# Performance work log

Hardware: AMD Instinct MI355X
Metric: run time of the kernel (lower is better)

## Reference

```python
import jax, jax.numpy as jnp
import numpy as np

H = 1024
B, S = 4, 2048
SCALE = 1.0 / np.sqrt(H)  # single-head: head_dim == hidden_dim


def setup_inputs() -> dict:
    key = jax.random.key(0)
    k1, k2, k3, k4 = jax.random.split(key, 4)
    inp = jax.random.normal(k1, (B, S, H), dtype=jnp.float32)
    # nn.Linear(h, h, bias=False) weights, stored [out, in]
    wq = jax.random.normal(k2, (H, H), dtype=jnp.float32) / np.sqrt(H)
    wk = jax.random.normal(k3, (H, H), dtype=jnp.float32) / np.sqrt(H)
    wv = jax.random.normal(k4, (H, H), dtype=jnp.float32) / np.sqrt(H)
    # causal mask, broadcast over batch: 1 = attend, 0 = masked
    attention_mask = jnp.broadcast_to(
        jnp.tril(jnp.ones((S, S), dtype=jnp.int32)), (B, S, S))
    return {"input": inp, "attention_mask": attention_mask,
            "wq": wq, "wk": wk, "wv": wv}


def reference(input, attention_mask, wq, wk, wv):
    # Linear: x @ W^T
    Q = jnp.einsum('bsh,oh->bso', input, wq)
    K = jnp.einsum('bsh,oh->bso', input, wk)
    V = jnp.einsum('bsh,oh->bso', input, wv)
    scores = jnp.einsum('bqh,bkh->bqk', Q, K) * SCALE  # [B,S,S]
    neg_inf = jnp.asarray(-jnp.inf, dtype=scores.dtype)
    scores = jnp.where(attention_mask == 0, neg_inf, scores)
    attn = jax.nn.softmax(scores, axis=-1)
    # dropout prob = 0.0 (eval): identity
    return jnp.einsum('bqk,bkh->bqh', attn, V)
```

## Files before the change

### kernel.cpp

```cpp
#include <hip/hip_runtime.h>
#include <hip/hip_bf16.h>
#include <stdint.h>

typedef __attribute__((ext_vector_type(8))) short short8;
typedef __attribute__((ext_vector_type(4))) float f32x4;
typedef __attribute__((ext_vector_type(4))) float fvec4;
typedef __attribute__((ext_vector_type(4))) unsigned short us4;

#define DEV static __device__ __forceinline__

constexpr int Hn = 1024;
constexpr int Bn = 4;
constexpr int Sn = 2048;
constexpr float SCALE_F = 0.03125f;
constexpr float LOG2E_F = 1.4426950408889634f;
constexpr float CEXP = SCALE_F * LOG2E_F;
constexpr int PTILES = 136;

DEV unsigned short f2bf(float f) {
  union { float f; unsigned u; } c; c.f = f;
  unsigned r = c.u + 0x7fffu + ((c.u >> 16) & 1u);
  return (unsigned short)(r >> 16);
}

DEV void gload16(const void* g, void* l) {
  __builtin_amdgcn_global_load_lds(
      (const __attribute__((address_space(1))) void*)g,
      (__attribute__((address_space(3))) void*)l, 16, 0, 0);
}

#define VMCNT(n) asm volatile("s_waitcnt vmcnt(" #n ")" ::: "memory")
#define LGKM0()  asm volatile("s_waitcnt lgkmcnt(0)" ::: "memory")
#define BAR()    asm volatile("s_barrier" ::: "memory")

DEV int swz_wg(int bid, int n) {
  const int q = n >> 3, r = n & 7, x = bid & 7, o = bid >> 3;
  return (x < r ? x * (q + 1) : r * (q + 1) + (x - r) * q) + o;
}

__global__ __launch_bounds__(256) void cvt_kernel(
    const float* __restrict__ x, const float* __restrict__ wq,
    const float* __restrict__ wk, const float* __restrict__ wv,
    unsigned short* __restrict__ xb, unsigned short* __restrict__ wb,
    float* __restrict__ lz) {
  if (blockIdx.x == 0) {
    f32x4 z = {0.f, 0.f, 0.f, 0.f};
    for (int i = threadIdx.x; i < Bn * Sn / 4; i += 256) ((f32x4*)lz)[i] = z;
  }
  const int NX4 = Bn * Sn * Hn / 4;
  const int NW4 = Hn * Hn / 4;
  const int total = NX4 + 3 * NW4;
  for (int i = blockIdx.x * 256 + threadIdx.x; i < total; i += gridDim.x * 256) {
    const fvec4* s; us4* d; int j;
    if (i < NX4)                { s = (const fvec4*)x;  d = (us4*)xb;             j = i; }
    else if (i < NX4 + NW4)     { s = (const fvec4*)wq; d = (us4*)wb;             j = i - NX4; }
    else if (i < NX4 + 2 * NW4) { s = (const fvec4*)wk; d = (us4*)(wb + Hn * Hn); j = i - NX4 - NW4; }
    else                        { s = (const fvec4*)wv; d = (us4*)(wb + 2 * Hn * Hn); j = i - NX4 - 2 * NW4; }
    fvec4 v = s[j];
    us4 o;
    o[0] = f2bf(v[0]); o[1] = f2bf(v[1]); o[2] = f2bf(v[2]); o[3] = f2bf(v[3]);
    d[j] = o;
  }
}

#define MFMA16(H, V, B) do {                                                     \
  __builtin_amdgcn_s_setprio(1);                                                 \
  _Pragma("unroll") for (int m_ = 0; m_ < 4; m_++)                               \
  _Pragma("unroll") for (int n_ = 0; n_ < 2; n_++)                               \
  _Pragma("unroll") for (int ks_ = 0; ks_ < 2; ks_++)                            \
    acc[H][V][m_][n_] = __builtin_amdgcn_mfma_f32_16x16x32_bf16(                 \
        afr[m_][ks_], (B)[n_][ks_], acc[H][V][m_][n_], 0, 0, 0);                 \
  __builtin_amdgcn_s_setprio(0);                                                 \
  __builtin_amdgcn_sched_barrier(0);                                             \
} while (0)

template <int MODE>
__global__ __launch_bounds__(512, 2) void gemm256_kernel(
    const unsigned short* __restrict__ A, int lda, int64_t a_bstride,
    const unsigned short* __restrict__ Bm, int ldb, int64_t b_bstride,
    unsigned short* __restrict__ C0, unsigned short* __restrict__ C1,
    float* __restrict__ lsum, int n_split, int ldc, int bm_mod, int K) {
  __shared__ __attribute__((aligned(16))) unsigned short LDSm[8][8192];
  char* lds = (char*)LDSm;
  const int tid = threadIdx.x, lane = tid & 63, wave = tid >> 6;
  const int wr = wave >> 2, wc = wave & 3;
  const int ln15 = lane & 15, hi = lane >> 4;

  int bm, bn, zl = 0;
  const int wg = swz_wg(blockIdx.x, gridDim.x);
  if (MODE == 0) { bm = wg % bm_mod; bn = wg / bm_mod; }
  else {
    zl = wg / 36;
    const int t = wg - zl * 36;
    bm = (int)((sqrtf(8.f * t + 1.f) - 1.f) * 0.5f);
    if (bm * (bm + 1) / 2 > t) bm--;
    if ((bm + 1) * (bm + 2) / 2 <= t) bm++;
    bn = t - bm * (bm + 1) / 2;
  }
  const unsigned short* Ab = A + (int64_t)zl * a_bstride;
  const unsigned short* Bb = Bm + (int64_t)zl * b_bstride;

  const int srow = tid >> 3;
  const int kch = ((tid & 7) ^ (srow & 7)) << 3;
  const unsigned short* Ag = Ab + (int64_t)(bm * 256 + srow) * lda + kch;
  const unsigned short* Bg = Bb + (int64_t)(bn * 256 + srow) * ldb + kch;
  const int dst_off = tid * 16;

  auto stageA = [&](int half, int t, int buf) {
    const unsigned short* s = Ag + (int64_t)(half * 128) * lda + (t << 6);
    char* d = lds + ((buf * 4 + half) << 14) + dst_off;
    gload16(s, d);
    gload16(s + (int64_t)64 * lda, d + 8192);
  };
  auto stageB = [&](int half, int t, int buf) {
    const unsigned short* s = Bg + (int64_t)(half * 128) * ldb + (t << 6);
    char* d = lds + ((buf * 4 + 2 + half) << 14) + dst_off;
    gload16(s, d);
    gload16(s + (int64_t)64 * ldb, d + 8192);
  };
  auto rdA = [&](int buf, int half, int rr, int ks) -> short8 {
    return *(const short8*)(lds + ((buf * 4 + half) << 14) + rr * 128 +
                            (((ks << 6) + (hi << 4)) ^ ((rr & 7) << 4)));
  };
  auto rdB = [&](int buf, int half, int rr, int ks) -> short8 {
    return *(const short8*)(lds + ((buf * 4 + 2 + half) << 14) + rr * 128 +
                            (((ks << 6) + (hi << 4)) ^ ((rr & 7) << 4)));
  };

  f32x4 acc[2][2][4][2];
#pragma unroll
  for (int h = 0; h < 2; h++)
#pragma unroll
    for (int v = 0; v < 2; v++)
#pragma unroll
      for (int m = 0; m < 4; m++)
#pragma unroll
        for (int n = 0; n < 2; n++) acc[h][v][m][n] = (f32x4){0.f, 0.f, 0.f, 0.f};

  short8 afr[4][2], b0r[2][2], b1r[2][2];

  stageA(0, 0, 0); stageB(0, 0, 0); stageB(1, 0, 0); stageA(1, 0, 0);
  VMCNT(4);
  BAR();

  const int nkt = K >> 6;
  for (int t = 0; t < nkt; ++t) {
    const int buf = t & 1, nb2 = buf ^ 1;
    const bool st = (t + 1 < nkt);
#pragma unroll
    for (int m = 0; m < 4; m++) {
      afr[m][0] = rdA(buf, 0, wr * 64 + m * 16 + ln15, 0);
      afr[m][1] = rdA(buf, 0, wr * 64 + m * 16 + ln15, 1);
    }
#pragma unroll
    for (int n = 0; n < 2; n++) {
      b0r[n][0] = rdB(buf, 0, wc * 32 + n * 16 + ln15, 0);
      b0r[n][1] = rdB(buf, 0, wc * 32 + n * 16 + ln15, 1);
    }
    if (st) { stageA(0, t + 1, nb2); VMCNT(4); } else { VMCNT(2); }
    BAR(); LGKM0(); __builtin_amdgcn_sched_barrier(0);
    MFMA16(0, 0, b0r);
    BAR();
#pragma unroll
    for (int n = 0; n < 2; n++) {
      b1r[n][0] = rdB(buf, 1, wc * 32 + n * 16 + ln15, 0);
      b1r[n][1] = rdB(buf, 1, wc * 32 + n * 16 + ln15, 1);
    }
    if (st) { stageB(0, t + 1, nb2); VMCNT(4); } else { VMCNT(0); }
    BAR(); LGKM0(); __builtin_amdgcn_sched_barrier(0);
    MFMA16(0, 1, b1r);
    BAR();
#pragma unroll
    for (int m = 0; m < 4; m++) {
      afr[m][0] = rdA(buf, 1, wr * 64 + m * 16 + ln15, 0);
      afr[m][1] = rdA(buf, 1, wr * 64 + m * 16 + ln15, 1);
    }
    if (st) { stageB(1, t + 1, nb2); VMCNT(6); } else { VMCNT(0); }
    BAR(); LGKM0(); __builtin_amdgcn_sched_barrier(0);
    MFMA16(1, 0, b0r);
    BAR();
    if (st) { stageA(1, t + 1, nb2); VMCNT(4); } else { VMCNT(0); }
    BAR();
    MFMA16(1, 1, b1r);
    BAR();
  }

  if (MODE == 0) {
#pragma unroll
    for (int h = 0; h < 2; h++)
#pragma unroll
      for (int v = 0; v < 2; v++)
#pragma unroll
        for (int n = 0; n < 2; n++) {
          int cc = bn * 256 + v * 128 + wc * 32 + n * 16;
          unsigned short* cb = C0;
          if (cc >= n_split) { cb = C1; cc -= n_split; }
          cc += ln15;
#pragma unroll
          for (int m = 0; m < 4; m++) {
            const int r0 = bm * 256 + h * 128 + wr * 64 + m * 16 + hi * 4;
#pragma unroll
            for (int j = 0; j < 4; j++)
              cb[(int64_t)(r0 + j) * ldc + cc] = f2bf(acc[h][v][m][n][j]);
          }
        }
  } else {
    unsigned short* Pb = C0 + (int64_t)zl * (PTILES * 16384);
    float* lb = lsum + zl * Sn;
#pragma unroll
    for (int h = 0; h < 2; h++)
#pragma unroll
      for (int m = 0; m < 4; m++)
#pragma unroll
        for (int j = 0; j < 4; j++) {
          const int row = bm * 256 + h * 128 + wr * 64 + m * 16 + hi * 4 + j;
          const int tq = row >> 7;
          float s = 0.f;
#pragma unroll
          for (int v = 0; v < 2; v++)
#pragma unroll
            for (int n = 0; n < 2; n++) {
              const int col = bn * 256 + v * 128 + wc * 32 + n * 16 + ln15;
              const float p =
                  (col <= row) ? __builtin_amdgcn_exp2f(acc[h][v][m][n][j] * CEXP) : 0.f;
              s += p;
              const int tk = col >> 7;
              if (tk <= tq)
                Pb[((int64_t)(tq * (tq + 1) / 2 + tk) << 14) + ((row & 127) << 7) +
                   (col & 127)] = f2bf(p);
            }
          s += __shfl_xor(s, 1); s += __shfl_xor(s, 2);
          s += __shfl_xor(s, 4); s += __shfl_xor(s, 8);
          if (ln15 == 0) atomicAdd(&lb[row], s);
        }
  }
}

__global__ __launch_bounds__(256) void pv_gemm_kernel(
    const unsigned short* __restrict__ Pp,
    const unsigned short* __restrict__ VTb,
    const float* __restrict__ l,
    float* __restrict__ Out) {
  const int w = blockIdx.x;
  const int bm = 15 - (w >> 5);
  const int inner = w & 31;
  const int bn = inner & 7;
  const int b = inner >> 3;

  __shared__ __attribute__((aligned(16))) unsigned short As[2][128 * 32];
  __shared__ __attribute__((aligned(16))) unsigned short Bs[2][128 * 32];
  const int tid = threadIdx.x, lane = tid & 63, wave = tid >> 6;
  const int wr = wave >> 1, wc = wave & 1;
  const int ln15 = lane & 15, hi = lane >> 4;

  const int arow = wave * 32 + (lane >> 2);
  const int aswz = (((lane & 3) ^ ((lane >> 2) & 3)) << 3);
  const unsigned short* Abase = Pp + (int64_t)b * (PTILES * 16384) +
      ((int64_t)(bm * (bm + 1) / 2) << 14) + (arow << 7) + aswz;
  const unsigned short* Bg = VTb + (int64_t)(bn * 128 + arow) * (Bn * Sn) +
      (int64_t)b * Sn + aswz;

  f32x4 acc[4][4];
#pragma unroll
  for (int m = 0; m < 4; m++)
#pragma unroll
    for (int n = 0; n < 4; n++) acc[m][n] = (f32x4){0.f, 0.f, 0.f, 0.f};

  auto stage = [&](int kt, int buf) {
    const unsigned short* a_src = Abase + ((int64_t)(kt >> 2) << 14) + (kt & 3) * 32;
    const unsigned short* b_src = Bg + kt * 32;
    char* a = (char*)As[buf] + wave * 2048;
    char* bl = (char*)Bs[buf] + wave * 2048;
    gload16(a_src, a);
    gload16(a_src + 2048, a + 1024);
    gload16(b_src, bl);
    gload16(b_src + (int64_t)16 * (Bn * Sn), bl + 1024);
  };

  const int nkt = (bm + 1) * 4;
  stage(0, 0);
  __syncthreads();
  for (int kt = 0; kt < nkt; ++kt) {
    const int buf = kt & 1;
    if (kt + 1 < nkt) stage(kt + 1, buf ^ 1);
    const char* Ap = (const char*)As[buf];
    const char* Bp = (const char*)Bs[buf];
    short8 af[4], bfv[4];
#pragma unroll
    for (int m = 0; m < 4; m++) {
      const int rr = wr * 64 + m * 16 + ln15;
      af[m] = *(const short8*)(Ap + rr * 64 + ((hi ^ (rr & 3)) << 4));
    }
#pragma unroll
    for (int n = 0; n < 4; n++) {
      const int rr = wc * 64 + n * 16 + ln15;
      bfv[n] = *(const short8*)(Bp + rr * 64 + ((hi ^ (rr & 3)) << 4));
    }
#pragma unroll
    for (int m = 0; m < 4; m++)
#pragma unroll
      for (int n = 0; n < 4; n++)
        acc[m][n] = __builtin_amdgcn_mfma_f32_16x16x32_bf16(af[m], bfv[n], acc[m][n], 0, 0, 0);
    __syncthreads();
  }

#pragma unroll
  for (int m = 0; m < 4; m++) {
    const int r0 = bm * 128 + wr * 64 + m * 16 + hi * 4;
#pragma unroll
    for (int j = 0; j < 4; j++) {
      const int q = r0 + j;
      const float linv = 1.0f / l[(int64_t)b * Sn + q];
#pragma unroll
      for (int n = 0; n < 4; n++) {
        const int d = bn * 128 + wc * 64 + n * 16 + ln15;
        Out[(int64_t)b * Sn * Hn + (int64_t)q * Hn + d] = acc[m][n][j] * linv;
      }
    }
  }
}

extern "C" void kernel_launch(void* const* d_in, const int* in_sizes, int n_in,
                              void* d_out, int out_size, void* d_ws, size_t ws_size,
                              hipStream_t stream) {
  const float* x  = (const float*)d_in[0];
  const float* wq = (const float*)d_in[2];
  const float* wk = (const float*)d_in[3];
  const float* wv = (const float*)d_in[4];
  float* out = (float*)d_out;
  char* ws = (char*)d_ws;

  const int64_t MiB = 1ll << 20;
  unsigned short* xb = (unsigned short*)(ws);
  unsigned short* wb = (unsigned short*)(ws + 16 * MiB);
  unsigned short* Pp = (unsigned short*)(ws);
  float* l           = (float*)(ws + 22 * MiB);
  unsigned short* Qb = (unsigned short*)(ws + 23 * MiB);
  unsigned short* Kb = (unsigned short*)(ws + 39 * MiB);
  unsigned short* VT = (unsigned short*)(ws + 55 * MiB);

  cvt_kernel<<<2048, 256, 0, stream>>>(x, wq, wk, wv, xb, wb, l);
  gemm256_kernel<0><<<256, 512, 0, stream>>>(
      xb, 1024, 0, wb, 1024, 0, Qb, Kb, nullptr, 1024, 1024, 32, 1024);
  gemm256_kernel<0><<<128, 512, 0, stream>>>(
      wb + 2 * 1024 * 1024, 1024, 0, xb, 1024, 0, VT, VT, nullptr, 1 << 30, 8192, 4, 1024);
  gemm256_kernel<1><<<144, 512, 0, stream>>>(
      Qb, 1024, (int64_t)Sn * Hn, Kb, 1024, (int64_t)Sn * Hn,
      Pp, nullptr, l, 1 << 30, 0, 0, 1024);
  pv_gemm_kernel<<<512, 256, 0, stream>>>(Pp, VT, l, out);
}
```

Measured before the change: 169.5 us.

## Deepen PV GEMM k-tile to 64, use vmcnt-based pipelining and XCD-aware block mapping

```diff
diff --git a/kernel.cpp b/kernel.cpp
--- a/kernel.cpp
+++ b/kernel.cpp
@@ -236,29 +236,43 @@
   }
 }
 
-__global__ __launch_bounds__(256) void pv_gemm_kernel(
+__global__ __launch_bounds__(256, 2) void pv_gemm_kernel(
     const unsigned short* __restrict__ Pp,
     const unsigned short* __restrict__ VTb,
     const float* __restrict__ l,
     float* __restrict__ Out) {
-  const int w = blockIdx.x;
-  const int bm = 15 - (w >> 5);
-  const int inner = w & 31;
+  const int xcd = blockIdx.x & 7;
+  const int inner = blockIdx.x >> 3;
   const int bn = inner & 7;
-  const int b = inner >> 3;
-
-  __shared__ __attribute__((aligned(16))) unsigned short As[2][128 * 32];
-  __shared__ __attribute__((aligned(16))) unsigned short Bs[2][128 * 32];
+  const int slot = inner >> 3;
+  const int r = slot * 8 + xcd;
+  const int bm = 15 - (r >> 2);
+  const int b = r & 3;
+
+  __shared__ __attribute__((aligned(16))) unsigned short As[2][128 * 64];
+  __shared__ __attribute__((aligned(16))) unsigned short Bs[2][128 * 64];
   const int tid = threadIdx.x, lane = tid & 63, wave = tid >> 6;
   const int wr = wave >> 1, wc = wave & 1;
   const int ln15 = lane & 15, hi = lane >> 4;
 
-  const int arow = wave * 32 + (lane >> 2);
-  const int aswz = (((lane & 3) ^ ((lane >> 2) & 3)) << 3);
-  const unsigned short* Abase = Pp + (int64_t)b * (PTILES * 16384) +
-      ((int64_t)(bm * (bm + 1) / 2) << 14) + (arow << 7) + aswz;
-  const unsigned short* Bg = VTb + (int64_t)(bn * 128 + arow) * (Bn * Sn) +
-      (int64_t)b * Sn + aswz;
+  const int srow0 = wave * 8 + (lane >> 3);
+  const int gch = (((lane & 7) ^ (srow0 & 7)) << 3);
+  const unsigned short* Pbase = Pp + (int64_t)b * (PTILES * 16384) +
+      ((int64_t)(bm * (bm + 1) / 2) << 14);
+  const unsigned short* Vbase = VTb + (int64_t)(bn * 128) * (Bn * Sn) + (int64_t)b * Sn;
+
+  auto stage = [&](int kt, int buf) {
+    char* a = (char*)As[buf] + wave * 1024;
+    char* bl = (char*)Bs[buf] + wave * 1024;
+    const int64_t a_off = ((int64_t)(kt >> 1) << 14) + (kt & 1) * 64 + gch;
+    const int64_t v_off = (int64_t)kt * 64 + gch;
+#pragma unroll
+    for (int j = 0; j < 4; ++j) {
+      const int row = srow0 + j * 32;
+      gload16(Pbase + a_off + ((int64_t)row << 7), a + j * 4096);
+      gload16(Vbase + v_off + (int64_t)row * (Bn * Sn), bl + j * 4096);
+    }
+  };
 
   f32x4 acc[4][4];
 #pragma unroll
@@ -266,42 +280,38 @@
 #pragma unroll
     for (int n = 0; n < 4; n++) acc[m][n] = (f32x4){0.f, 0.f, 0.f, 0.f};
 
-  auto stage = [&](int kt, int buf) {
-    const unsigned short* a_src = Abase + ((int64_t)(kt >> 2) << 14) + (kt & 3) * 32;
-    const unsigned short* b_src = Bg + kt * 32;
-    char* a = (char*)As[buf] + wave * 2048;
-    char* bl = (char*)Bs[buf] + wave * 2048;
-    gload16(a_src, a);
-    gload16(a_src + 2048, a + 1024);
-    gload16(b_src, bl);
-    gload16(b_src + (int64_t)16 * (Bn * Sn), bl + 1024);
-  };
-
-  const int nkt = (bm + 1) * 4;
+  const int nkt = (bm + 1) * 2;
   stage(0, 0);
-  __syncthreads();
   for (int kt = 0; kt < nkt; ++kt) {
     const int buf = kt & 1;
-    if (kt + 1 < nkt) stage(kt + 1, buf ^ 1);
+    if (kt + 1 < nkt) { stage(kt + 1, buf ^ 1); VMCNT(8); }
+    else { VMCNT(0); }
+    BAR();
     const char* Ap = (const char*)As[buf];
     const char* Bp = (const char*)Bs[buf];
-    short8 af[4], bfv[4];
+    short8 af[4][2], bf[4][2];
 #pragma unroll
     for (int m = 0; m < 4; m++) {
       const int rr = wr * 64 + m * 16 + ln15;
-      af[m] = *(const short8*)(Ap + rr * 64 + ((hi ^ (rr & 3)) << 4));
+#pragma unroll
+      for (int ks = 0; ks < 2; ks++)
+        af[m][ks] = *(const short8*)(Ap + rr * 128 + (((ks << 6) + (hi << 4)) ^ ((rr & 7) << 4)));
     }
 #pragma unroll
     for (int n = 0; n < 4; n++) {
       const int rr = wc * 64 + n * 16 + ln15;
-      bfv[n] = *(const short8*)(Bp + rr * 64 + ((hi ^ (rr & 3)) << 4));
-    }
-#pragma unroll
-    for (int m = 0; m < 4; m++)
-#pragma unroll
-      for (int n = 0; n < 4; n++)
-        acc[m][n] = __builtin_amdgcn_mfma_f32_16x16x32_bf16(af[m], bfv[n], acc[m][n], 0, 0, 0);
-    __syncthreads();
+#pragma unroll
+      for (int ks = 0; ks < 2; ks++)
+        bf[n][ks] = *(const short8*)(Bp + rr * 128 + (((ks << 6) + (hi << 4)) ^ ((rr & 7) << 4)));
+    }
+#pragma unroll
+    for (int ks = 0; ks < 2; ks++)
+#pragma unroll
+      for (int m = 0; m < 4; m++)
+#pragma unroll
+        for (int n = 0; n < 4; n++)
+          acc[m][n] = __builtin_amdgcn_mfma_f32_16x16x32_bf16(af[m][ks], bf[n][ks], acc[m][n], 0, 0, 0);
+    BAR();
   }
 
 #pragma unroll
```

New measurement: 158.9 us. 1.07x faster.
